# Kernel optimization log

Measured on AMD Instinct MI355X. Metric: run time of the kernel, lower is better.

## Reference

```python
import jax, jax.numpy as jnp
import numpy as np

B, T = 32, 64
I, O, H = 64, 64, 512
N, W = 128, 64           # memory slots, slot width
IF = 3 * W + 6           # interface size


def setup_inputs() -> dict:
    key = jax.random.key(0)
    ks = jax.random.split(key, 6)
    s = 0.05
    return {
        "x": jax.random.normal(ks[0], (B, T, I), jnp.float32),
        "W_ih": jax.random.normal(ks[1], (4 * H, I + W), jnp.float32) * s,
        "W_hh": jax.random.normal(ks[2], (4 * H, H), jnp.float32) * s,
        "b_ih": jnp.zeros((4 * H,), jnp.float32),
        "b_hh": jnp.zeros((4 * H,), jnp.float32),
        "W_if": jax.random.normal(ks[3], (IF, H), jnp.float32) * s,
        "b_if": jnp.zeros((IF,), jnp.float32),
        "W_out": jax.random.normal(ks[4], (O, H + W), jnp.float32) * s,
        "b_out": jnp.zeros((O,), jnp.float32),
    }


def reference(x, W_ih, W_hh, b_ih, b_hh, W_if, b_if, W_out, b_out):
    Bb, Tt, _ = x.shape
    dt = x.dtype
    eye = jnp.eye(N, dtype=dt)
    batch_idx = jnp.arange(Bb)[:, None]

    def step(carry, x_t):
        h, c, mem, usage, prec, link, rw, rvec = carry
        # --- LSTM controller (PyTorch gate order i,f,g,o) ---
        inp = jnp.concatenate([x_t, rvec], axis=-1)
        gates = inp @ W_ih.T + h @ W_hh.T + b_ih + b_hh
        i_g, f_g, g_g, o_g = jnp.split(gates, 4, axis=-1)
        c = jax.nn.sigmoid(f_g) * c + jax.nn.sigmoid(i_g) * jnp.tanh(g_g)
        h = jax.nn.sigmoid(o_g) * jnp.tanh(c)
        itf = h @ W_if.T + b_if
        # --- parse interface ---
        erase = jax.nn.sigmoid(itf[:, :W])
        wvec = itf[:, W:2 * W]
        wg = jax.nn.sigmoid(itf[:, 2 * W])
        ag = jax.nn.sigmoid(itf[:, 2 * W + 1])
        rstr = jnp.log1p(jnp.exp(itf[:, 3 * W + 2]))  # softplus
        # --- allocation weighting (sort usage asc, shifted cumprod, scatter) ---
        idx = jnp.argsort(usage, axis=-1)
        usage_sorted = jnp.take_along_axis(usage, idx, axis=-1)
        cprod = jnp.cumprod(usage_sorted, axis=-1)
        cprod = jnp.concatenate([jnp.ones((Bb, 1), dt), cprod[:, :-1]], axis=-1)
        alloc_in_order = (1.0 - usage_sorted) * cprod
        alloc = jnp.zeros_like(usage).at[batch_idx, idx].set(alloc_in_order)
        ww = wg[:, None] * ag[:, None] * alloc  # [B,N]
        # --- erase + add write ---
        mem = mem * (1.0 - ww[:, :, None] * erase[:, None, :]) + ww[:, :, None] * wvec[:, None, :]
        usage = usage + (1.0 - usage) * ww
        # --- temporal link / precedence ---
        ww_ij = ww[:, :, None] + ww[:, None, :]
        link = (1.0 - ww_ij) * link + prec[:, :, None] * ww[:, None, :]
        link = link * (1.0 - eye)
        prec = (1.0 - ww.sum(-1, keepdims=True)) * prec + ww
        # --- read weights (NOTE: source uses itf[:, :W] as read key) ---
        rmode = jax.nn.softmax(itf[:, -3:], axis=-1)
        rkey = itf[:, :W]
        dot = jnp.einsum('bw,bnw->bn', rkey, mem)
        kn = jnp.linalg.norm(rkey, axis=-1, keepdims=True) + 1e-8
        mn = jnp.linalg.norm(mem, axis=-1) + 1e-8
        cw = jax.nn.softmax(dot / (kn * mn) * rstr[:, None], axis=-1)
        bw = jnp.einsum('bnm,bn->bm', link, rw)   # link^T @ rw
        fw = jnp.einsum('bnm,bm->bn', link, rw)   # link @ rw
        wts = rmode[:, 0:1] * bw + rmode[:, 1:2] * fw + rmode[:, 2:3] * cw + 1e-8
        wts = wts / wts.sum(-1, keepdims=True)
        rvec = jnp.einsum('bn,bnw->bw', wts, mem)
        out = jnp.concatenate([h, rvec], axis=-1) @ W_out.T + b_out
        return (h, c, mem, usage, prec, link, wts, rvec), out

    z = lambda *s: jnp.zeros(s, dt)
    carry0 = (z(Bb, H), z(Bb, H), z(Bb, N, W), z(Bb, N), z(Bb, N), z(Bb, N, N), z(Bb, N), z(Bb, W))
    _, outs = jax.lax.scan(step, carry0, jnp.swapaxes(x, 0, 1))
    return jnp.swapaxes(outs, 0, 1)  # [B,T,O]
```

## Files before the change

kernel.cpp:

```cpp
#include <hip/hip_runtime.h>
#include <math.h>

#define Bb 32
#define Tt 64
#define Ii 64
#define Oo 64
#define Hh 512
#define Nn 128
#define Wd 64
#define IFs 198
#define KV 640
#define G4 2048

#define NP1 128
#define NWG 160
#define NT 512

#define P2_MEM    0
#define P2_H      8320
#define P2_SCR    8896
#define P2_ITF    10944
#define P2_ERASE  11168
#define P2_WVEC   11232
#define P2_USAGE  11296
#define P2_PREC   11424
#define P2_RW     11552
#define P2_WW     11680
#define P2_SCAN   11808
#define P2_SS     11936
#define P2_SCAL   12064
#define P2_BIF    12080
#define P2_ALLOC  12304
#define P1_WIF    0
#define P1_BS     13464
#define P1_V      13720
#define P1_CC     15016
#define P1_HSL    15144
#define P1_PACC   15272
#define SMEM_FLOATS 23592
#define SMEM_BYTES (SMEM_FLOATS * 4)

#define S_WWSUM 0

__device__ __align__(16) float g_WT[KV * G4];
__device__ __align__(16) float g_bsum[G4];
typedef unsigned long long u64;
__device__ u64 g_h64[2 * Bb * Hh];
__device__ u64 g_rv64[Bb * Wd];
__device__ u64 g_if64[Bb * 8 * 200];

__device__ __forceinline__ float sigf(float v) { return 1.f / (1.f + expf(-v)); }

__device__ __forceinline__ u64 ldrelax(const u64* p) {
  return __hip_atomic_load(p, __ATOMIC_RELAXED, __HIP_MEMORY_SCOPE_AGENT);
}
__device__ __forceinline__ void tstore(u64* p, unsigned tag, float v) {
  u64 val = ((u64)tag << 32) | (u64)__float_as_uint(v);
  __hip_atomic_store(p, val, __ATOMIC_RELAXED, __HIP_MEMORY_SCOPE_AGENT);
}
__device__ __forceinline__ float fixwait(const u64* p, u64 v, unsigned tag) {
  while ((unsigned)(v >> 32) != tag) {
    __builtin_amdgcn_s_sleep(1);
    v = ldrelax(p);
  }
  return __uint_as_float((unsigned)(v & 0xffffffffu));
}

#define TIN 512
__global__ __launch_bounds__(TIN) void dnc_init(const float* __restrict__ W_ih,
                                                const float* __restrict__ W_hh,
                                                const float* __restrict__ b_ih,
                                                const float* __restrict__ b_hh) {
  __shared__ float tile[64][65];
  const int tid = threadIdx.x;
  int i0 = blockIdx.x * blockDim.x + tid;
  int st = gridDim.x * blockDim.x;
  for (int idx = i0; idx < G4; idx += st) g_bsum[idx] = b_ih[idx] + b_hh[idx];
  for (int idx = i0; idx < 2 * Bb * Hh; idx += st) g_h64[idx] = 0ull;
  for (int idx = i0; idx < Bb * Wd; idx += st) g_rv64[idx] = 0ull;
  for (int idx = i0; idx < Bb * 8 * 200; idx += st) g_if64[idx] = 0ull;

  for (int tileId = blockIdx.x; tileId < 320; tileId += gridDim.x) {
    int tc = tileId >> 5, tj = tileId & 31;
    for (int k = tid; k < 64 * 64; k += TIN) {
      int r = k >> 6, cl = k & 63;
      int j = tj * 64 + r, c = tc * 64 + cl;
      tile[r][cl] = (c < 128) ? W_ih[j * 128 + c] : W_hh[j * 512 + (c - 128)];
    }
    __syncthreads();
    for (int k = tid; k < 64 * 64; k += TIN) {
      int cl = k >> 6, rjj = k & 63;
      int c = tc * 64 + cl;
      int rp = (c < 128) ? (512 + c) : (c - 128);
      g_WT[(size_t)rp * G4 + tj * 64 + rjj] = tile[rjj][cl];
    }
    __syncthreads();
  }
}

__global__ __launch_bounds__(NT) void dnc_main(const float* __restrict__ x,
                                               const float* __restrict__ W_if,
                                               const float* __restrict__ b_if,
                                               const float* __restrict__ W_out,
                                               const float* __restrict__ b_out,
                                               float* __restrict__ out) {
  extern __shared__ float sm[];
  const int tid = threadIdx.x;
  const int wg = blockIdx.x;

  if (wg < NP1) {
    const int jb = wg & 7;
    const int bb = wg >> 3;
    const int b0 = bb * 2;
    for (int i = tid; i < IFs * 64; i += NT) {
      int o = i >> 6, c = i & 63;
      sm[P1_WIF + o * 68 + c] = W_if[(size_t)o * Hh + jb * 64 + c];
    }
    if (tid < 64) {
      int gq = tid >> 4, m = tid & 15;
      ((float4*)(sm + P1_BS))[tid] = ((const float4*)g_bsum)[gq * 128 + jb * 16 + m];
    }
    if (tid < 128) sm[P1_CC + tid] = 0.f;
    __syncthreads();

    for (int t = 0; t < Tt; ++t) {
      {
        const u64* hsrc = g_h64 + (size_t)((t + 1) & 1) * (Bb * Hh);
        const int u = tid;
        const u64* a0 = hsrc + (size_t)b0 * Hh + u;
        const u64* a1 = hsrc + (size_t)(b0 + 1) * Hh + u;
        u64 v0 = ldrelax(a0), v1 = ldrelax(a1);
        float2 hh;
        hh.x = fixwait(a0, v0, (unsigned)t);
        hh.y = fixwait(a1, v1, (unsigned)t);
        *(float2*)(sm + P1_V + u * 2) = hh;
        if (tid < 128) {
          const int bl2 = tid >> 6, i = tid & 63;
          float xv = x[((size_t)(b0 + bl2) * Tt + t) * Ii + i];
          sm[P1_V + (512 + i) * 2 + bl2] = xv;
        }
      }
      __syncthreads();

      {
        const int fg = tid & 31, ks = tid >> 5;
        const int fcolA = ((fg >> 4) * 128) + jb * 16 + (fg & 15);
        const float* v2 = sm + P1_V + ks * 80;
        const float4* wpA = (const float4*)g_WT + (size_t)(ks * 40) * 512 + fcolA;
        if (ks >= 14) {
          const int j = tid & 63;
          const u64* r0 = g_rv64 + (size_t)b0 * Wd + j;
          const u64* r1 = g_rv64 + (size_t)(b0 + 1) * Wd + j;
          u64 u0 = ldrelax(r0), u1 = ldrelax(r1);
          float2 rv;
          rv.x = fixwait(r0, u0, (unsigned)t);
          rv.y = fixwait(r1, u1, (unsigned)t);
          *(float2*)(sm + P1_V + (576 + j) * 2) = rv;
        }
        float4 aA0 = {0.f, 0.f, 0.f, 0.f}, aA1 = {0.f, 0.f, 0.f, 0.f};
        float4 aB0 = {0.f, 0.f, 0.f, 0.f}, aB1 = {0.f, 0.f, 0.f, 0.f};
#pragma unroll 4
        for (int r = 0; r < 40; ++r) {
          float4 wA = wpA[(size_t)r * 512];
          float4 wB = wpA[(size_t)r * 512 + 256];
          float2 vv = *(const float2*)(v2 + r * 2);
          aA0.x += wA.x * vv.x; aA0.y += wA.y * vv.x; aA0.z += wA.z * vv.x; aA0.w += wA.w * vv.x;
          aA1.x += wA.x * vv.y; aA1.y += wA.y * vv.y; aA1.z += wA.z * vv.y; aA1.w += wA.w * vv.y;
          aB0.x += wB.x * vv.x; aB0.y += wB.y * vv.x; aB0.z += wB.z * vv.x; aB0.w += wB.w * vv.x;
          aB1.x += wB.x * vv.y; aB1.y += wB.y * vv.y; aB1.z += wB.z * vv.y; aB1.w += wB.w * vv.y;
        }
        float4* pacc = (float4*)(sm + P1_PACC);
        pacc[(ks * 2 + 0) * 65 + fg] = aA0;
        pacc[(ks * 2 + 1) * 65 + fg] = aA1;
        pacc[(ks * 2 + 0) * 65 + fg + 32] = aB0;
        pacc[(ks * 2 + 1) * 65 + fg + 32] = aB1;
      }
      __syncthreads();
      if (tid < 128) {
        const int bl = tid >> 6, l = tid & 63;
        const float* pb = sm + P1_PACC + bl * 260 + l;
        float gv0 = 0.f, gv1 = 0.f, gv2 = 0.f, gv3 = 0.f;
#pragma unroll
        for (int ks = 0; ks < 16; ++ks) {
          const float* pk = pb + ks * 520;
          gv0 += pk[0];
          gv1 += pk[64];
          gv2 += pk[128];
          gv3 += pk[192];
        }
        float ig = gv0 + sm[P1_BS + l];
        float fg = gv1 + sm[P1_BS + 64 + l];
        float gg = gv2 + sm[P1_BS + 128 + l];
        float og = gv3 + sm[P1_BS + 192 + l];
        float co = sm[P1_CC + bl * 64 + l];
        float cn = sigf(fg) * co + sigf(ig) * tanhf(gg);
        float hn = sigf(og) * tanhf(cn);
        sm[P1_CC + bl * 64 + l] = cn;
        sm[P1_HSL + bl * 64 + l] = hn;
        tstore(g_h64 + (size_t)(t & 1) * (Bb * Hh) + (size_t)(b0 + bl) * Hh + jb * 64 + l,
               (unsigned)(t + 1), hn);
      }
      __syncthreads();
      if (tid < 2 * IFs) {
        const int o = tid >> 1, bl = tid & 1;
        const float4* wr = (const float4*)(sm + P1_WIF + o * 68);
        const float4* h4 = (const float4*)(sm + P1_HSL + bl * 64);
        float acc = 0.f;
#pragma unroll 8
        for (int c4 = 0; c4 < 16; ++c4) {
          float4 w = wr[c4]; float4 h = h4[c4];
          acc += w.x * h.x + w.y * h.y + w.z * h.z + w.w * h.w;
        }
        tstore(g_if64 + ((size_t)(b0 + bl) * 8 + jb) * 200 + o, (unsigned)(t + 1), acc);
      }
    }
  } else {
    const int b = wg - NP1;
    float* SCR = sm + P2_SCR;
    float regL[32], regLT[32];
#pragma unroll
    for (int k = 0; k < 32; ++k) { regL[k] = 0.f; regLT[k] = 0.f; }
    for (int i = tid; i < Nn * 65; i += NT) sm[P2_MEM + i] = 0.f;
    if (tid < 128) { sm[P2_USAGE + tid] = 0.f; sm[P2_PREC + tid] = 0.f; sm[P2_RW + tid] = 0.f; }
    if (tid < IFs) sm[P2_BIF + tid] = b_if[tid];
    __syncthreads();
    if (tid < 64) {
      const int li = tid, i0 = 2 * li, i1 = i0 + 1;
      float u0 = sm[P2_USAGE + i0], u1 = sm[P2_USAGE + i1];
      int r0 = 0, r1 = 0;
      for (int jc = 0; jc < 32; ++jc) {
        float4 uj4 = *(const float4*)(sm + P2_USAGE + jc * 4);
#pragma unroll
        for (int e = 0; e < 4; ++e) {
          float uj = (&uj4.x)[e];
          int j = jc * 4 + e;
          r0 += (uj < u0 || (uj == u0 && j < i0)) ? 1 : 0;
          r1 += (uj < u1 || (uj == u1 && j < i1)) ? 1 : 0;
        }
      }
      sm[P2_SS + r0] = u0;
      sm[P2_SS + r1] = u1;
      float s0 = sm[P2_SS + i0], s1 = sm[P2_SS + i1];
      float p = s0 * s1;
#pragma unroll
      for (int off = 1; off < 64; off <<= 1) {
        float v = __shfl_up(p, off, 64);
        if (li >= off) p *= v;
      }
      float E = __shfl_up(p, 1, 64);
      if (li == 0) E = 1.f;
      sm[P2_SCAN + i0] = E * s0;
      sm[P2_SCAN + i1] = E * s0 * s1;
      float ex0 = (r0 > 0) ? sm[P2_SCAN + r0 - 1] : 1.f;
      float ex1 = (r1 > 0) ? sm[P2_SCAN + r1 - 1] : 1.f;
      sm[P2_ALLOC + i0] = (1.f - u0) * ex0;
      sm[P2_ALLOC + i1] = (1.f - u1) * ex1;
    }
    __syncthreads();

    for (int t = 0; t < Tt; ++t) {
      if (tid < 2 * IFs) {
        const int o = tid >> 1, hf = tid & 1;
        const u64* src = g_if64 + ((size_t)b * 8 + hf * 4) * 200 + o;
        u64 a0 = ldrelax(src), a1 = ldrelax(src + 200),
            a2 = ldrelax(src + 400), a3 = ldrelax(src + 600);
        float s = fixwait(src, a0, (unsigned)(t + 1))
                + fixwait(src + 200, a1, (unsigned)(t + 1))
                + fixwait(src + 400, a2, (unsigned)(t + 1))
                + fixwait(src + 600, a3, (unsigned)(t + 1));
        s += __shfl_xor(s, 1, 64);
        if (hf == 0) sm[P2_ITF + o] = s + sm[P2_BIF + o];
      }
      __syncthreads();
      float kn_r = 0.f, rstr_r = 0.f, rm0_r = 0.f, rm1_r = 0.f, rm2_r = 0.f;
      if (tid < 64) {
        const int li = tid, i0 = 2 * li, i1 = i0 + 1;
        float wgag = sigf(sm[P2_ITF + 128]) * sigf(sm[P2_ITF + 129]);
        float rs = sm[P2_ITF + 194];
        rstr_r = (rs > 20.f) ? rs : log1pf(expf(rs));
        float m0 = sm[P2_ITF + 195], m1 = sm[P2_ITF + 196], m2 = sm[P2_ITF + 197];
        float mx = fmaxf(m0, fmaxf(m1, m2));
        float e0 = expf(m0 - mx), e1 = expf(m1 - mx), e2 = expf(m2 - mx);
        float es = e0 + e1 + e2;
        rm0_r = e0 / es; rm1_r = e1 / es; rm2_r = e2 / es;
        float rk = sm[P2_ITF + li];
        sm[P2_ERASE + li] = sigf(rk);
        sm[P2_WVEC + li] = sm[P2_ITF + 64 + li];
        float sq = rk * rk;
#pragma unroll
        for (int off = 32; off > 0; off >>= 1) sq += __shfl_xor(sq, off, 64);
        kn_r = sqrtf(sq) + 1e-8f;
        float u0 = sm[P2_USAGE + i0], u1 = sm[P2_USAGE + i1];
        float w0 = wgag * sm[P2_ALLOC + i0];
        float w1 = wgag * sm[P2_ALLOC + i1];
        sm[P2_WW + i0] = w0; sm[P2_WW + i1] = w1;
        sm[P2_USAGE + i0] = u0 + (1.f - u0) * w0;
        sm[P2_USAGE + i1] = u1 + (1.f - u1) * w1;
        float wws = w0 + w1;
#pragma unroll
        for (int off = 32; off > 0; off >>= 1) wws += __shfl_xor(wws, off, 64);
        if (li == 0) sm[P2_SCAL + S_WWSUM] = wws;
      }
      __syncthreads();
      {
        const int n = tid & 127, ws = tid >> 7;
        float4 er[4], wv[4], kf[4];
#pragma unroll
        for (int r = 0; r < 4; ++r) {
          er[r] = *(const float4*)(sm + P2_ERASE + ws * 16 + r * 4);
          wv[r] = *(const float4*)(sm + P2_WVEC + ws * 16 + r * 4);
          kf[r] = *(const float4*)(sm + P2_ITF + ws * 16 + r * 4);
        }
        float wwn = sm[P2_WW + n];
        float dotp = 0.f, mnp = 0.f;
        const int base = P2_MEM + n * 65 + ws * 16;
#pragma unroll
        for (int q = 0; q < 16; ++q) {
          float m = sm[base + q];
          float ee = (&er[q >> 2].x)[q & 3];
          float vv = (&wv[q >> 2].x)[q & 3];
          float kk = (&kf[q >> 2].x)[q & 3];
          m = m * (1.f - wwn * ee) + wwn * vv;
          sm[base + q] = m;
          dotp += kk * m;
          mnp += m * m;
        }
        SCR[ws * 128 + n] = dotp;
        SCR[512 + ws * 128 + n] = mnp;
        const int m = n, ns = ws;
        float wwm = wwn;
        float prn = sm[P2_PREC + m];
        float bwp = 0.f, fwp = 0.f;
#pragma unroll
        for (int kq = 0; kq < 8; ++kq) {
          float4 ww4 = *(const float4*)(sm + P2_WW + ns * 32 + kq * 4);
          float4 pr4 = *(const float4*)(sm + P2_PREC + ns * 32 + kq * 4);
          float4 rw4 = *(const float4*)(sm + P2_RW + ns * 32 + kq * 4);
#pragma unroll
          for (int e = 0; e < 4; ++e) {
            int k = kq * 4 + e;
            int nn = ns * 32 + k;
            float wwo = (&ww4.x)[e];
            float pro = (&pr4.x)[e];
            float rwo = (&rw4.x)[e];
            float L = regL[k];
            L = (1.f - wwo - wwm) * L + pro * wwm;
            if (nn == m) L = 0.f;
            regL[k] = L;
            bwp += L * rwo;
            float LT = regLT[k];
            LT = (1.f - wwm - wwo) * LT + prn * wwo;
            if (nn == m) LT = 0.f;
            regLT[k] = LT;
            fwp += LT * rwo;
          }
        }
        SCR[1024 + ns * 128 + m] = bwp;
        SCR[1536 + ns * 128 + m] = fwp;
      }
      __syncthreads();
      if (tid < 64) {
        int i0 = 2 * tid, i1 = i0 + 1;
        float d0 = SCR[i0] + SCR[128 + i0] + SCR[256 + i0] + SCR[384 + i0];
        float d1 = SCR[i1] + SCR[128 + i1] + SCR[256 + i1] + SCR[384 + i1];
        float mn0 = sqrtf(SCR[512 + i0] + SCR[640 + i0] + SCR[768 + i0] + SCR[896 + i0]) + 1e-8f;
        float mn1 = sqrtf(SCR[512 + i1] + SCR[640 + i1] + SCR[768 + i1] + SCR[896 + i1]) + 1e-8f;
        float bw0 = SCR[1024 + i0] + SCR[1152 + i0] + SCR[1280 + i0] + SCR[1408 + i0];
        float bw1 = SCR[1024 + i1] + SCR[1152 + i1] + SCR[1280 + i1] + SCR[1408 + i1];
        float fw0 = SCR[1536 + i0] + SCR[1664 + i0] + SCR[1792 + i0] + SCR[1920 + i0];
        float fw1 = SCR[1536 + i1] + SCR[1664 + i1] + SCR[1792 + i1] + SCR[1920 + i1];
        float q0 = d0 / (kn_r * mn0) * rstr_r;
        float q1 = d1 / (kn_r * mn1) * rstr_r;
        float mx = fmaxf(q0, q1);
#pragma unroll
        for (int off = 32; off > 0; off >>= 1) mx = fmaxf(mx, __shfl_xor(mx, off, 64));
        float e0 = expf(q0 - mx), e1 = expf(q1 - mx);
        float es = e0 + e1;
#pragma unroll
        for (int off = 32; off > 0; off >>= 1) es += __shfl_xor(es, off, 64);
        float wv0 = rm0_r * bw0 + rm1_r * fw0 + rm2_r * (e0 / es) + 1e-8f;
        float wv1 = rm0_r * bw1 + rm1_r * fw1 + rm2_r * (e1 / es) + 1e-8f;
        float wsum = wv0 + wv1;
#pragma unroll
        for (int off = 32; off > 0; off >>= 1) wsum += __shfl_xor(wsum, off, 64);
        sm[P2_RW + i0] = wv0 / wsum;
        sm[P2_RW + i1] = wv1 / wsum;
      }
      __syncthreads();
      {
        const int w = tid & 63, ns8 = tid >> 6;
        float4 rw4[4];
#pragma unroll
        for (int r = 0; r < 4; ++r)
          rw4[r] = *(const float4*)(sm + P2_RW + ns8 * 16 + r * 4);
        float p = 0.f;
#pragma unroll
        for (int k = 0; k < 16; ++k)
          p += (&rw4[k >> 2].x)[k & 3] * sm[P2_MEM + (ns8 * 16 + k) * 65 + w];
        SCR[ns8 * 64 + w] = p;
      }
      __syncthreads();
      if (tid < 64) {
        float r = 0.f;
#pragma unroll
        for (int s2 = 0; s2 < 8; ++s2) r += SCR[s2 * 64 + tid];
        sm[P2_H + 512 + tid] = r;
        tstore(g_rv64 + (size_t)b * Wd + tid, (unsigned)(t + 1), r);
      } else if (tid < 320) {
        const int idx = tid - 64;
        const u64* hsrc = g_h64 + (size_t)(t & 1) * (Bb * Hh) + (size_t)b * Hh;
        const u64* a0 = hsrc + idx * 2;
        const u64* a1 = hsrc + idx * 2 + 1;
        u64 v0 = ldrelax(a0), v1 = ldrelax(a1);
        sm[P2_H + idx * 2] = fixwait(a0, v0, (unsigned)(t + 1));
        sm[P2_H + idx * 2 + 1] = fixwait(a1, v1, (unsigned)(t + 1));
      } else if (tid < 384) {
        const int li = tid - 320, i0 = 2 * li, i1 = i0 + 1;
        float u0 = sm[P2_USAGE + i0], u1 = sm[P2_USAGE + i1];
        int r0 = 0, r1 = 0;
        for (int jc = 0; jc < 32; ++jc) {
          float4 uj4 = *(const float4*)(sm + P2_USAGE + jc * 4);
#pragma unroll
          for (int e = 0; e < 4; ++e) {
            float uj = (&uj4.x)[e];
            int j = jc * 4 + e;
            r0 += (uj < u0 || (uj == u0 && j < i0)) ? 1 : 0;
            r1 += (uj < u1 || (uj == u1 && j < i1)) ? 1 : 0;
          }
        }
        sm[P2_SS + r0] = u0;
        sm[P2_SS + r1] = u1;
        float s0 = sm[P2_SS + i0], s1 = sm[P2_SS + i1];
        float p = s0 * s1;
#pragma unroll
        for (int off = 1; off < 64; off <<= 1) {
          float v = __shfl_up(p, off, 64);
          if (li >= off) p *= v;
        }
        float E = __shfl_up(p, 1, 64);
        if (li == 0) E = 1.f;
        sm[P2_SCAN + i0] = E * s0;
        sm[P2_SCAN + i1] = E * s0 * s1;
        float ex0 = (r0 > 0) ? sm[P2_SCAN + r0 - 1] : 1.f;
        float ex1 = (r1 > 0) ? sm[P2_SCAN + r1 - 1] : 1.f;
        sm[P2_ALLOC + i0] = (1.f - u0) * ex0;
        sm[P2_ALLOC + i1] = (1.f - u1) * ex1;
      } else {
        const int n = tid - 384;
        float wws = sm[P2_SCAL + S_WWSUM];
        sm[P2_PREC + n] = (1.f - wws) * sm[P2_PREC + n] + sm[P2_WW + n];
      }
      __syncthreads();
      {
        const int o = tid >> 3, seg = tid & 7;
        const float4* wrow = (const float4*)(W_out + (size_t)o * 576) + seg * 18;
        const float4* hb = (const float4*)(sm + P2_H) + seg * 18;
        float p = 0.f;
#pragma unroll
        for (int q = 0; q < 18; ++q) {
          float4 w = wrow[q]; float4 h = hb[q];
          p += w.x * h.x + w.y * h.y + w.z * h.z + w.w * h.w;
        }
        p += __shfl_down(p, 4, 8);
        p += __shfl_down(p, 2, 8);
        p += __shfl_down(p, 1, 8);
        if (seg == 0) out[((size_t)b * Tt + t) * Oo + o] = p + b_out[o];
      }
    }
  }
}

extern "C" void kernel_launch(void* const* d_in, const int* in_sizes, int n_in,
                              void* d_out, int out_size, void* d_ws, size_t ws_size,
                              hipStream_t stream) {
  (void)in_sizes; (void)n_in; (void)d_ws; (void)ws_size; (void)out_size;
  const float* x    = (const float*)d_in[0];
  const float* W_ih = (const float*)d_in[1];
  const float* W_hh = (const float*)d_in[2];
  const float* b_ih = (const float*)d_in[3];
  const float* b_hh = (const float*)d_in[4];
  const float* W_if = (const float*)d_in[5];
  const float* b_if = (const float*)d_in[6];
  const float* W_out = (const float*)d_in[7];
  const float* b_out = (const float*)d_in[8];
  float* out = (float*)d_out;

  dnc_init<<<320, TIN, 0, stream>>>(W_ih, W_hh, b_ih, b_hh);

  hipFuncSetAttribute((const void*)dnc_main,
                      hipFuncAttributeMaxDynamicSharedMemorySize, SMEM_BYTES);

  void* args[] = {(void*)&x, (void*)&W_if, (void*)&b_if,
                  (void*)&W_out, (void*)&b_out, (void*)&out};
  hipLaunchCooperativeKernel((void*)dnc_main, dim3(NWG), dim3(NT), args,
                             SMEM_BYTES, stream);
}
```

Baseline: 873.5 us.

## Merge LSTM and memory stages into uniform per-batch workgroups with redundant memory updates

Replaces the split of 128 LSTM workgroups plus 32 memory workgroups with 256 uniform workgroups. Each handles one batch element and one slice of hidden units, and each redundantly keeps its own copy of the DNC memory, link and usage state. This removes the cross-workgroup read-vector handoff (g_rv64) and the dedicated memory stage from the critical path. Each group now gathers the interface vector from the 8 partial sums and runs the full memory update locally, and the output projection is deferred by one step and spread across groups. In exchange it does 8x redundant memory work, uses more shared memory per group (launch bounds set to 2 groups per CU), and reuses each weight load for only one batch row instead of two.

```diff
diff --git a/kernel.cpp b/kernel.cpp
--- a/kernel.cpp
+++ b/kernel.cpp
@@ -12,41 +12,36 @@
 #define KV 640
 #define G4 2048
 
-#define NP1 128
-#define NWG 160
+#define NWG 256
 #define NT 512
 
-#define P2_MEM    0
-#define P2_H      8320
-#define P2_SCR    8896
-#define P2_ITF    10944
-#define P2_ERASE  11168
-#define P2_WVEC   11232
-#define P2_USAGE  11296
-#define P2_PREC   11424
-#define P2_RW     11552
-#define P2_WW     11680
-#define P2_SCAN   11808
-#define P2_SS     11936
-#define P2_SCAL   12064
-#define P2_BIF    12080
-#define P2_ALLOC  12304
-#define P1_WIF    0
-#define P1_BS     13464
-#define P1_V      13720
-#define P1_CC     15016
-#define P1_HSL    15144
-#define P1_PACC   15272
-#define SMEM_FLOATS 23592
+#define L_WIF    0
+#define L_BS     13464
+#define L_V      13720
+#define L_CC     14360
+#define L_HSL    14424
+#define L_BIF    14488
+#define L_ITF    14712
+#define L_ERASE  14936
+#define L_WVEC   15000
+#define L_USAGE  15064
+#define L_PREC   15192
+#define L_RW     15320
+#define L_WW     15448
+#define L_SCAN   15576
+#define L_SS     15704
+#define L_ALLOC  15832
+#define L_SCAL   15960
+#define L_SCR    15976
+#define L_PACC   18024
+#define L_MEM    22184
+#define SMEM_FLOATS 30504
 #define SMEM_BYTES (SMEM_FLOATS * 4)
-
-#define S_WWSUM 0
 
 __device__ __align__(16) float g_WT[KV * G4];
 __device__ __align__(16) float g_bsum[G4];
 typedef unsigned long long u64;
 __device__ u64 g_h64[2 * Bb * Hh];
-__device__ u64 g_rv64[Bb * Wd];
 __device__ u64 g_if64[Bb * 8 * 200];
 
 __device__ __forceinline__ float sigf(float v) { return 1.f / (1.f + expf(-v)); }
@@ -77,7 +72,6 @@
   int st = gridDim.x * blockDim.x;
   for (int idx = i0; idx < G4; idx += st) g_bsum[idx] = b_ih[idx] + b_hh[idx];
   for (int idx = i0; idx < 2 * Bb * Hh; idx += st) g_h64[idx] = 0ull;
-  for (int idx = i0; idx < Bb * Wd; idx += st) g_rv64[idx] = 0ull;
   for (int idx = i0; idx < Bb * 8 * 200; idx += st) g_if64[idx] = 0ull;
 
   for (int tileId = blockIdx.x; tileId < 320; tileId += gridDim.x) {
@@ -98,138 +92,319 @@
   }
 }
 
-__global__ __launch_bounds__(NT) void dnc_main(const float* __restrict__ x,
-                                               const float* __restrict__ W_if,
-                                               const float* __restrict__ b_if,
-                                               const float* __restrict__ W_out,
-                                               const float* __restrict__ b_out,
-                                               float* __restrict__ out) {
+__global__ __launch_bounds__(NT, 2) void dnc_main(const float* __restrict__ x,
+                                                  const float* __restrict__ W_if,
+                                                  const float* __restrict__ b_if,
+                                                  const float* __restrict__ W_out,
+                                                  const float* __restrict__ b_out,
+                                                  float* __restrict__ out) {
   extern __shared__ float sm[];
   const int tid = threadIdx.x;
   const int wg = blockIdx.x;
-
-  if (wg < NP1) {
-    const int jb = wg & 7;
-    const int bb = wg >> 3;
-    const int b0 = bb * 2;
-    for (int i = tid; i < IFs * 64; i += NT) {
-      int o = i >> 6, c = i & 63;
-      sm[P1_WIF + o * 68 + c] = W_if[(size_t)o * Hh + jb * 64 + c];
-    }
+  const int jb = wg & 7;
+  const int b = wg >> 3;
+
+  float regL[32], regLT[32];
+#pragma unroll
+  for (int k = 0; k < 32; ++k) { regL[k] = 0.f; regLT[k] = 0.f; }
+
+  for (int i = tid; i < IFs * 64; i += NT) {
+    int o = i >> 6, c = i & 63;
+    sm[L_WIF + o * 68 + c] = W_if[(size_t)o * Hh + jb * 64 + c];
+  }
+  if (tid < 64) {
+    int gq = tid >> 4, m = tid & 15;
+    ((float4*)(sm + L_BS))[tid] = ((const float4*)g_bsum)[gq * 128 + jb * 16 + m];
+    sm[L_CC + tid] = 0.f;
+    sm[L_V + 576 + tid] = 0.f;
+  }
+  if (tid < IFs) sm[L_BIF + tid] = b_if[tid];
+  if (tid < 128) {
+    sm[L_USAGE + tid] = 0.f;
+    sm[L_PREC + tid] = 0.f;
+    sm[L_RW + tid] = 0.f;
+  }
+  for (int i = tid; i < Nn * 65; i += NT) sm[L_MEM + i] = 0.f;
+  __syncthreads();
+  if (tid < 64) {
+    const int li = tid, i0 = 2 * li, i1 = i0 + 1;
+    float u0 = sm[L_USAGE + i0], u1 = sm[L_USAGE + i1];
+    int r0 = 0, r1 = 0;
+    for (int jc = 0; jc < 32; ++jc) {
+      float4 uj4 = *(const float4*)(sm + L_USAGE + jc * 4);
+#pragma unroll
+      for (int e = 0; e < 4; ++e) {
+        float uj = (&uj4.x)[e];
+        int j = jc * 4 + e;
+        r0 += (uj < u0 || (uj == u0 && j < i0)) ? 1 : 0;
+        r1 += (uj < u1 || (uj == u1 && j < i1)) ? 1 : 0;
+      }
+    }
+    sm[L_SS + r0] = u0;
+    sm[L_SS + r1] = u1;
+    float s0 = sm[L_SS + i0], s1 = sm[L_SS + i1];
+    float p = s0 * s1;
+#pragma unroll
+    for (int off = 1; off < 64; off <<= 1) {
+      float v = __shfl_up(p, off, 64);
+      if (li >= off) p *= v;
+    }
+    float E = __shfl_up(p, 1, 64);
+    if (li == 0) E = 1.f;
+    sm[L_SCAN + i0] = E * s0;
+    sm[L_SCAN + i1] = E * s0 * s1;
+    float ex0 = (r0 > 0) ? sm[L_SCAN + r0 - 1] : 1.f;
+    float ex1 = (r1 > 0) ? sm[L_SCAN + r1 - 1] : 1.f;
+    sm[L_ALLOC + i0] = (1.f - u0) * ex0;
+    sm[L_ALLOC + i1] = (1.f - u1) * ex1;
+  }
+  __syncthreads();
+
+  for (int t = 0; t < Tt; ++t) {
+    {
+      const u64* a0 = g_h64 + (size_t)((t + 1) & 1) * (Bb * Hh) + (size_t)b * Hh + tid;
+      u64 v0 = ldrelax(a0);
+      sm[L_V + tid] = fixwait(a0, v0, (unsigned)t);
+      if (tid < 64) sm[L_V + 512 + tid] = x[((size_t)b * Tt + t) * Ii + tid];
+    }
+    __syncthreads();
+    {
+      const int fg = tid & 31, ks = tid >> 5;
+      const int fcolA = ((fg >> 4) * 128) + jb * 16 + (fg & 15);
+      const float* va = sm + L_V + ks * 40;
+      const float4* wpA = (const float4*)g_WT + (size_t)(ks * 40) * 512 + fcolA;
+      float4 aA = {0.f, 0.f, 0.f, 0.f}, aB = {0.f, 0.f, 0.f, 0.f};
+#pragma unroll 4
+      for (int r = 0; r < 40; ++r) {
+        float4 wA = wpA[(size_t)r * 512];
+        float4 wB = wpA[(size_t)r * 512 + 256];
+        float fv = va[r];
+        aA.x += wA.x * fv; aA.y += wA.y * fv; aA.z += wA.z * fv; aA.w += wA.w * fv;
+        aB.x += wB.x * fv; aB.y += wB.y * fv; aB.z += wB.z * fv; aB.w += wB.w * fv;
+      }
+      float4* pacc = (float4*)(sm + L_PACC);
+      pacc[ks * 65 + fg] = aA;
+      pacc[ks * 65 + fg + 32] = aB;
+    }
+    __syncthreads();
     if (tid < 64) {
-      int gq = tid >> 4, m = tid & 15;
-      ((float4*)(sm + P1_BS))[tid] = ((const float4*)g_bsum)[gq * 128 + jb * 16 + m];
-    }
-    if (tid < 128) sm[P1_CC + tid] = 0.f;
-    __syncthreads();
-
-    for (int t = 0; t < Tt; ++t) {
-      {
-        const u64* hsrc = g_h64 + (size_t)((t + 1) & 1) * (Bb * Hh);
-        const int u = tid;
-        const u64* a0 = hsrc + (size_t)b0 * Hh + u;
-        const u64* a1 = hsrc + (size_t)(b0 + 1) * Hh + u;
-        u64 v0 = ldrelax(a0), v1 = ldrelax(a1);
-        float2 hh;
-        hh.x = fixwait(a0, v0, (unsigned)t);
-        hh.y = fixwait(a1, v1, (unsigned)t);
-        *(float2*)(sm + P1_V + u * 2) = hh;
-        if (tid < 128) {
-          const int bl2 = tid >> 6, i = tid & 63;
-          float xv = x[((size_t)(b0 + bl2) * Tt + t) * Ii + i];
-          sm[P1_V + (512 + i) * 2 + bl2] = xv;
-        }
-      }
-      __syncthreads();
-
-      {
-        const int fg = tid & 31, ks = tid >> 5;
-        const int fcolA = ((fg >> 4) * 128) + jb * 16 + (fg & 15);
-        const float* v2 = sm + P1_V + ks * 80;
-        const float4* wpA = (const float4*)g_WT + (size_t)(ks * 40) * 512 + fcolA;
-        if (ks >= 14) {
-          const int j = tid & 63;
-          const u64* r0 = g_rv64 + (size_t)b0 * Wd + j;
-          const u64* r1 = g_rv64 + (size_t)(b0 + 1) * Wd + j;
-          u64 u0 = ldrelax(r0), u1 = ldrelax(r1);
-          float2 rv;
-          rv.x = fixwait(r0, u0, (unsigned)t);
-          rv.y = fixwait(r1, u1, (unsigned)t);
-          *(float2*)(sm + P1_V + (576 + j) * 2) = rv;
-        }
-        float4 aA0 = {0.f, 0.f, 0.f, 0.f}, aA1 = {0.f, 0.f, 0.f, 0.f};
-        float4 aB0 = {0.f, 0.f, 0.f, 0.f}, aB1 = {0.f, 0.f, 0.f, 0.f};
-#pragma unroll 4
-        for (int r = 0; r < 40; ++r) {
-          float4 wA = wpA[(size_t)r * 512];
-          float4 wB = wpA[(size_t)r * 512 + 256];
-          float2 vv = *(const float2*)(v2 + r * 2);
-          aA0.x += wA.x * vv.x; aA0.y += wA.y * vv.x; aA0.z += wA.z * vv.x; aA0.w += wA.w * vv.x;
-          aA1.x += wA.x * vv.y; aA1.y += wA.y * vv.y; aA1.z += wA.z * vv.y; aA1.w += wA.w * vv.y;
-          aB0.x += wB.x * vv.x; aB0.y += wB.y * vv.x; aB0.z += wB.z * vv.x; aB0.w += wB.w * vv.x;
-          aB1.x += wB.x * vv.y; aB1.y += wB.y * vv.y; aB1.z += wB.z * vv.y; aB1.w += wB.w * vv.y;
-        }
-        float4* pacc = (float4*)(sm + P1_PACC);
-        pacc[(ks * 2 + 0) * 65 + fg] = aA0;
-        pacc[(ks * 2 + 1) * 65 + fg] = aA1;
-        pacc[(ks * 2 + 0) * 65 + fg + 32] = aB0;
-        pacc[(ks * 2 + 1) * 65 + fg + 32] = aB1;
-      }
-      __syncthreads();
-      if (tid < 128) {
-        const int bl = tid >> 6, l = tid & 63;
-        const float* pb = sm + P1_PACC + bl * 260 + l;
-        float gv0 = 0.f, gv1 = 0.f, gv2 = 0.f, gv3 = 0.f;
-#pragma unroll
-        for (int ks = 0; ks < 16; ++ks) {
-          const float* pk = pb + ks * 520;
-          gv0 += pk[0];
-          gv1 += pk[64];
-          gv2 += pk[128];
-          gv3 += pk[192];
-        }
-        float ig = gv0 + sm[P1_BS + l];
-        float fg = gv1 + sm[P1_BS + 64 + l];
-        float gg = gv2 + sm[P1_BS + 128 + l];
-        float og = gv3 + sm[P1_BS + 192 + l];
-        float co = sm[P1_CC + bl * 64 + l];
-        float cn = sigf(fg) * co + sigf(ig) * tanhf(gg);
-        float hn = sigf(og) * tanhf(cn);
-        sm[P1_CC + bl * 64 + l] = cn;
-        sm[P1_HSL + bl * 64 + l] = hn;
-        tstore(g_h64 + (size_t)(t & 1) * (Bb * Hh) + (size_t)(b0 + bl) * Hh + jb * 64 + l,
-               (unsigned)(t + 1), hn);
-      }
-      __syncthreads();
-      if (tid < 2 * IFs) {
-        const int o = tid >> 1, bl = tid & 1;
-        const float4* wr = (const float4*)(sm + P1_WIF + o * 68);
-        const float4* h4 = (const float4*)(sm + P1_HSL + bl * 64);
-        float acc = 0.f;
-#pragma unroll 8
-        for (int c4 = 0; c4 < 16; ++c4) {
-          float4 w = wr[c4]; float4 h = h4[c4];
-          acc += w.x * h.x + w.y * h.y + w.z * h.z + w.w * h.w;
-        }
-        tstore(g_if64 + ((size_t)(b0 + bl) * 8 + jb) * 200 + o, (unsigned)(t + 1), acc);
-      }
-    }
-  } else {
-    const int b = wg - NP1;
-    float* SCR = sm + P2_SCR;
-    float regL[32], regLT[32];
-#pragma unroll
-    for (int k = 0; k < 32; ++k) { regL[k] = 0.f; regLT[k] = 0.f; }
-    for (int i = tid; i < Nn * 65; i += NT) sm[P2_MEM + i] = 0.f;
-    if (tid < 128) { sm[P2_USAGE + tid] = 0.f; sm[P2_PREC + tid] = 0.f; sm[P2_RW + tid] = 0.f; }
-    if (tid < IFs) sm[P2_BIF + tid] = b_if[tid];
-    __syncthreads();
+      const int l = tid;
+      const float* pb = sm + L_PACC + l;
+      float gv0 = 0.f, gv1 = 0.f, gv2 = 0.f, gv3 = 0.f;
+#pragma unroll
+      for (int ks = 0; ks < 16; ++ks) {
+        const float* pk = pb + ks * 260;
+        gv0 += pk[0];
+        gv1 += pk[64];
+        gv2 += pk[128];
+        gv3 += pk[192];
+      }
+      float ig = gv0 + sm[L_BS + l];
+      float fg = gv1 + sm[L_BS + 64 + l];
+      float gg = gv2 + sm[L_BS + 128 + l];
+      float og = gv3 + sm[L_BS + 192 + l];
+      float co = sm[L_CC + l];
+      float cn = sigf(fg) * co + sigf(ig) * tanhf(gg);
+      float hn = sigf(og) * tanhf(cn);
+      sm[L_CC + l] = cn;
+      sm[L_HSL + l] = hn;
+      tstore(g_h64 + (size_t)(t & 1) * (Bb * Hh) + (size_t)b * Hh + jb * 64 + l,
+             (unsigned)(t + 1), hn);
+    }
+    __syncthreads();
+    if (tid < 2 * IFs) {
+      const int o = tid >> 1, hf = tid & 1;
+      const float4* wr = (const float4*)(sm + L_WIF + o * 68) + hf * 8;
+      const float4* h4 = (const float4*)(sm + L_HSL) + hf * 8;
+      float acc = 0.f;
+#pragma unroll
+      for (int c4 = 0; c4 < 8; ++c4) {
+        float4 w = wr[c4]; float4 h = h4[c4];
+        acc += w.x * h.x + w.y * h.y + w.z * h.z + w.w * h.w;
+      }
+      acc += __shfl_xor(acc, 1, 64);
+      if (hf == 0)
+        tstore(g_if64 + ((size_t)b * 8 + jb) * 200 + o, (unsigned)(t + 1), acc);
+    }
+    const u64 *pp0, *pp1, *pp2, *pp3;
+    u64 pv0 = 0, pv1 = 0, pv2 = 0, pv3 = 0;
+    if (tid < 2 * IFs) {
+      const int o = tid >> 1, hf = tid & 1;
+      const u64* base = g_if64 + (size_t)b * 8 * 200 + (size_t)hf * 4 * 200 + o;
+      pp0 = base; pp1 = base + 200; pp2 = base + 400; pp3 = base + 600;
+      pv0 = ldrelax(pp0); pv1 = ldrelax(pp1); pv2 = ldrelax(pp2); pv3 = ldrelax(pp3);
+    }
+    if (t > 0 && tid >= 448) {
+      const int o8 = (tid - 448) >> 3, seg = tid & 7;
+      const int o = jb * 8 + o8;
+      const float4* w4 = (const float4*)(W_out + (size_t)o * 576) + seg * 18;
+      float p = 0.f;
+#pragma unroll
+      for (int q = 0; q < 18; ++q) {
+        float4 w = w4[q];
+        int v = seg * 72 + q * 4;
+        int r0 = (v < 512) ? v : v + 64;
+        p += w.x * sm[L_V + r0] + w.y * sm[L_V + r0 + 1]
+           + w.z * sm[L_V + r0 + 2] + w.w * sm[L_V + r0 + 3];
+      }
+      p += __shfl_down(p, 4, 8);
+      p += __shfl_down(p, 2, 8);
+      p += __shfl_down(p, 1, 8);
+      if (seg == 0) out[((size_t)b * Tt + (t - 1)) * Oo + o] = p + b_out[o];
+    }
+    if (tid < 2 * IFs) {
+      const int o = tid >> 1, hf = tid & 1;
+      float s = fixwait(pp0, pv0, (unsigned)(t + 1))
+              + fixwait(pp1, pv1, (unsigned)(t + 1))
+              + fixwait(pp2, pv2, (unsigned)(t + 1))
+              + fixwait(pp3, pv3, (unsigned)(t + 1));
+      s += __shfl_xor(s, 1, 64);
+      if (hf == 0) sm[L_ITF + o] = s + sm[L_BIF + o];
+    }
+    __syncthreads();
+    float kn_r = 0.f, rstr_r = 0.f, rm0_r = 0.f, rm1_r = 0.f, rm2_r = 0.f;
     if (tid < 64) {
       const int li = tid, i0 = 2 * li, i1 = i0 + 1;
-      float u0 = sm[P2_USAGE + i0], u1 = sm[P2_USAGE + i1];
+      float wgag = sigf(sm[L_ITF + 128]) * sigf(sm[L_ITF + 129]);
+      float rs = sm[L_ITF + 194];
+      rstr_r = (rs > 20.f) ? rs : log1pf(expf(rs));
+      float m0 = sm[L_ITF + 195], m1 = sm[L_ITF + 196], m2 = sm[L_ITF + 197];
+      float mx = fmaxf(m0, fmaxf(m1, m2));
+      float e0 = expf(m0 - mx), e1 = expf(m1 - mx), e2 = expf(m2 - mx);
+      float es = e0 + e1 + e2;
+      rm0_r = e0 / es; rm1_r = e1 / es; rm2_r = e2 / es;
+      float rk = sm[L_ITF + li];
+      sm[L_ERASE + li] = sigf(rk);
+      sm[L_WVEC + li] = sm[L_ITF + 64 + li];
+      float sq = rk * rk;
+#pragma unroll
+      for (int off = 32; off > 0; off >>= 1) sq += __shfl_xor(sq, off, 64);
+      kn_r = sqrtf(sq) + 1e-8f;
+      float u0 = sm[L_USAGE + i0], u1 = sm[L_USAGE + i1];
+      float w0 = wgag * sm[L_ALLOC + i0];
+      float w1 = wgag * sm[L_ALLOC + i1];
+      sm[L_WW + i0] = w0; sm[L_WW + i1] = w1;
+      sm[L_USAGE + i0] = u0 + (1.f - u0) * w0;
+      sm[L_USAGE + i1] = u1 + (1.f - u1) * w1;
+      float wws = w0 + w1;
+#pragma unroll
+      for (int off = 32; off > 0; off >>= 1) wws += __shfl_xor(wws, off, 64);
+      if (li == 0) sm[L_SCAL] = wws;
+    }
+    __syncthreads();
+    {
+      float* SCR = sm + L_SCR;
+      const int n = tid & 127, ws = tid >> 7;
+      float4 er[4], wv[4], kf[4];
+#pragma unroll
+      for (int r = 0; r < 4; ++r) {
+        er[r] = *(const float4*)(sm + L_ERASE + ws * 16 + r * 4);
+        wv[r] = *(const float4*)(sm + L_WVEC + ws * 16 + r * 4);
+        kf[r] = *(const float4*)(sm + L_ITF + ws * 16 + r * 4);
+      }
+      float wwn = sm[L_WW + n];
+      float dotp = 0.f, mnp = 0.f;
+      const int base = L_MEM + n * 65 + ws * 16;
+#pragma unroll
+      for (int q = 0; q < 16; ++q) {
+        float m = sm[base + q];
+        float ee = (&er[q >> 2].x)[q & 3];
+        float vv = (&wv[q >> 2].x)[q & 3];
+        float kk = (&kf[q >> 2].x)[q & 3];
+        m = m * (1.f - wwn * ee) + wwn * vv;
+        sm[base + q] = m;
+        dotp += kk * m;
+        mnp += m * m;
+      }
+      SCR[ws * 128 + n] = dotp;
+      SCR[512 + ws * 128 + n] = mnp;
+      const int m = n, ns = ws;
+      float wwm = wwn;
+      float prn = sm[L_PREC + m];
+      float bwp = 0.f, fwp = 0.f;
+#pragma unroll
+      for (int kq = 0; kq < 8; ++kq) {
+        float4 ww4 = *(const float4*)(sm + L_WW + ns * 32 + kq * 4);
+        float4 pr4 = *(const float4*)(sm + L_PREC + ns * 32 + kq * 4);
+        float4 rw4 = *(const float4*)(sm + L_RW + ns * 32 + kq * 4);
+#pragma unroll
+        for (int e = 0; e < 4; ++e) {
+          int k = kq * 4 + e;
+          int nn = ns * 32 + k;
+          float wwo = (&ww4.x)[e];
+          float pro = (&pr4.x)[e];
+          float rwo = (&rw4.x)[e];
+          float L = regL[k];
+          L = (1.f - wwo - wwm) * L + pro * wwm;
+          if (nn == m) L = 0.f;
+          regL[k] = L;
+          bwp += L * rwo;
+          float LT = regLT[k];
+          LT = (1.f - wwm - wwo) * LT + prn * wwo;
+          if (nn == m) LT = 0.f;
+          regLT[k] = LT;
+          fwp += LT * rwo;
+        }
+      }
+      SCR[1024 + ns * 128 + m] = bwp;
+      SCR[1536 + ns * 128 + m] = fwp;
+    }
+    __syncthreads();
+    if (tid < 64) {
+      float* SCR = sm + L_SCR;
+      int i0 = 2 * tid, i1 = i0 + 1;
+      float d0 = SCR[i0] + SCR[128 + i0] + SCR[256 + i0] + SCR[384 + i0];
+      float d1 = SCR[i1] + SCR[128 + i1] + SCR[256 + i1] + SCR[384 + i1];
+      float mn0 = sqrtf(SCR[512 + i0] + SCR[640 + i0] + SCR[768 + i0] + SCR[896 + i0]) + 1e-8f;
+      float mn1 = sqrtf(SCR[512 + i1] + SCR[640 + i1] + SCR[768 + i1] + SCR[896 + i1]) + 1e-8f;
+      float bw0 = SCR[1024 + i0] + SCR[1152 + i0] + SCR[1280 + i0] + SCR[1408 + i0];
+      float bw1 = SCR[1024 + i1] + SCR[1152 + i1] + SCR[1280 + i1] + SCR[1408 + i1];
+      float fw0 = SCR[1536 + i0] + SCR[1664 + i0] + SCR[1792 + i0] + SCR[1920 + i0];
+      float fw1 = SCR[1536 + i1] + SCR[1664 + i1] + SCR[1792 + i1] + SCR[1920 + i1];
+      float q0 = d0 / (kn_r * mn0) * rstr_r;
+      float q1 = d1 / (kn_r * mn1) * rstr_r;
+      float mx = fmaxf(q0, q1);
+#pragma unroll
+      for (int off = 32; off > 0; off >>= 1) mx = fmaxf(mx, __shfl_xor(mx, off, 64));
+      float e0 = expf(q0 - mx), e1 = expf(q1 - mx);
+      float es = e0 + e1;
+#pragma unroll
+      for (int off = 32; off > 0; off >>= 1) es += __shfl_xor(es, off, 64);
+      float wv0 = rm0_r * bw0 + rm1_r * fw0 + rm2_r * (e0 / es) + 1e-8f;
+      float wv1 = rm0_r * bw1 + rm1_r * fw1 + rm2_r * (e1 / es) + 1e-8f;
+      float wsum = wv0 + wv1;
+#pragma unroll
+      for (int off = 32; off > 0; off >>= 1) wsum += __shfl_xor(wsum, off, 64);
+      sm[L_RW + i0] = wv0 / wsum;
+      sm[L_RW + i1] = wv1 / wsum;
+    }
+    __syncthreads();
+    {
+      float* SCR = sm + L_SCR;
+      const int w = tid & 63, ns8 = tid >> 6;
+      float4 rw4[4];
+#pragma unroll
+      for (int r = 0; r < 4; ++r)
+        rw4[r] = *(const float4*)(sm + L_RW + ns8 * 16 + r * 4);
+      float p = 0.f;
+#pragma unroll
+      for (int k = 0; k < 16; ++k)
+        p += (&rw4[k >> 2].x)[k & 3] * sm[L_MEM + (ns8 * 16 + k) * 65 + w];
+      SCR[ns8 * 64 + w] = p;
+    }
+    __syncthreads();
+    if (tid < 64) {
+      const float* SCR = sm + L_SCR;
+      float r = 0.f;
+#pragma unroll
+      for (int s2 = 0; s2 < 8; ++s2) r += SCR[s2 * 64 + tid];
+      sm[L_V + 576 + tid] = r;
+    } else if (tid < 128) {
+      const int li = tid - 64, i0 = 2 * li, i1 = i0 + 1;
+      float u0 = sm[L_USAGE + i0], u1 = sm[L_USAGE + i1];
       int r0 = 0, r1 = 0;
       for (int jc = 0; jc < 32; ++jc) {
-        float4 uj4 = *(const float4*)(sm + P2_USAGE + jc * 4);
+        float4 uj4 = *(const float4*)(sm + L_USAGE + jc * 4);
 #pragma unroll
         for (int e = 0; e < 4; ++e) {
           float uj = (&uj4.x)[e];
@@ -238,9 +413,9 @@
           r1 += (uj < u1 || (uj == u1 && j < i1)) ? 1 : 0;
         }
       }
-      sm[P2_SS + r0] = u0;
-      sm[P2_SS + r1] = u1;
-      float s0 = sm[P2_SS + i0], s1 = sm[P2_SS + i1];
+      sm[L_SS + r0] = u0;
+      sm[L_SS + r1] = u1;
+      float s0 = sm[L_SS + i0], s1 = sm[L_SS + i1];
       float p = s0 * s1;
 #pragma unroll
       for (int off = 1; off < 64; off <<= 1) {
@@ -249,224 +424,42 @@
       }
       float E = __shfl_up(p, 1, 64);
       if (li == 0) E = 1.f;
-      sm[P2_SCAN + i0] = E * s0;
-      sm[P2_SCAN + i1] = E * s0 * s1;
-      float ex0 = (r0 > 0) ? sm[P2_SCAN + r0 - 1] : 1.f;
-      float ex1 = (r1 > 0) ? sm[P2_SCAN + r1 - 1] : 1.f;
-      sm[P2_ALLOC + i0] = (1.f - u0) * ex0;
-      sm[P2_ALLOC + i1] = (1.f - u1) * ex1;
-    }
-    __syncthreads();
-
-    for (int t = 0; t < Tt; ++t) {
-      if (tid < 2 * IFs) {
-        const int o = tid >> 1, hf = tid & 1;
-        const u64* src = g_if64 + ((size_t)b * 8 + hf * 4) * 200 + o;
-        u64 a0 = ldrelax(src), a1 = ldrelax(src + 200),
-            a2 = ldrelax(src + 400), a3 = ldrelax(src + 600);
-        float s = fixwait(src, a0, (unsigned)(t + 1))
-                + fixwait(src + 200, a1, (unsigned)(t + 1))
-                + fixwait(src + 400, a2, (unsigned)(t + 1))
-                + fixwait(src + 600, a3, (unsigned)(t + 1));
-        s += __shfl_xor(s, 1, 64);
-        if (hf == 0) sm[P2_ITF + o] = s + sm[P2_BIF + o];
-      }
-      __syncthreads();
-      float kn_r = 0.f, rstr_r = 0.f, rm0_r = 0.f, rm1_r = 0.f, rm2_r = 0.f;
-      if (tid < 64) {
-        const int li = tid, i0 = 2 * li, i1 = i0 + 1;
-        float wgag = sigf(sm[P2_ITF + 128]) * sigf(sm[P2_ITF + 129]);
-        float rs = sm[P2_ITF + 194];
-        rstr_r = (rs > 20.f) ? rs : log1pf(expf(rs));
-        float m0 = sm[P2_ITF + 195], m1 = sm[P2_ITF + 196], m2 = sm[P2_ITF + 197];
-        float mx = fmaxf(m0, fmaxf(m1, m2));
-        float e0 = expf(m0 - mx), e1 = expf(m1 - mx), e2 = expf(m2 - mx);
-        float es = e0 + e1 + e2;
-        rm0_r = e0 / es; rm1_r = e1 / es; rm2_r = e2 / es;
-        float rk = sm[P2_ITF + li];
-        sm[P2_ERASE + li] = sigf(rk);
-        sm[P2_WVEC + li] = sm[P2_ITF + 64 + li];
-        float sq = rk * rk;
-#pragma unroll
-        for (int off = 32; off > 0; off >>= 1) sq += __shfl_xor(sq, off, 64);
-        kn_r = sqrtf(sq) + 1e-8f;
-        float u0 = sm[P2_USAGE + i0], u1 = sm[P2_USAGE + i1];
-        float w0 = wgag * sm[P2_ALLOC + i0];
-        float w1 = wgag * sm[P2_ALLOC + i1];
-        sm[P2_WW + i0] = w0; sm[P2_WW + i1] = w1;
-        sm[P2_USAGE + i0] = u0 + (1.f - u0) * w0;
-        sm[P2_USAGE + i1] = u1 + (1.f - u1) * w1;
-        float wws = w0 + w1;
-#pragma unroll
-        for (int off = 32; off > 0; off >>= 1) wws += __shfl_xor(wws, off, 64);
-        if (li == 0) sm[P2_SCAL + S_WWSUM] = wws;
-      }
-      __syncthreads();
-      {
-        const int n = tid & 127, ws = tid >> 7;
-        float4 er[4], wv[4], kf[4];
-#pragma unroll
-        for (int r = 0; r < 4; ++r) {
-          er[r] = *(const float4*)(sm + P2_ERASE + ws * 16 + r * 4);
-          wv[r] = *(const float4*)(sm + P2_WVEC + ws * 16 + r * 4);
-          kf[r] = *(const float4*)(sm + P2_ITF + ws * 16 + r * 4);
-        }
-        float wwn = sm[P2_WW + n];
-        float dotp = 0.f, mnp = 0.f;
-        const int base = P2_MEM + n * 65 + ws * 16;
-#pragma unroll
-        for (int q = 0; q < 16; ++q) {
-          float m = sm[base + q];
-          float ee = (&er[q >> 2].x)[q & 3];
-          float vv = (&wv[q >> 2].x)[q & 3];
-          float kk = (&kf[q >> 2].x)[q & 3];
-          m = m * (1.f - wwn * ee) + wwn * vv;
-          sm[base + q] = m;
-          dotp += kk * m;
-          mnp += m * m;
-        }
-        SCR[ws * 128 + n] = dotp;
-        SCR[512 + ws * 128 + n] = mnp;
-        const int m = n, ns = ws;
-        float wwm = wwn;
-        float prn = sm[P2_PREC + m];
-        float bwp = 0.f, fwp = 0.f;
-#pragma unroll
-        for (int kq = 0; kq < 8; ++kq) {
-          float4 ww4 = *(const float4*)(sm + P2_WW + ns * 32 + kq * 4);
-          float4 pr4 = *(const float4*)(sm + P2_PREC + ns * 32 + kq * 4);
-          float4 rw4 = *(const float4*)(sm + P2_RW + ns * 32 + kq * 4);
-#pragma unroll
-          for (int e = 0; e < 4; ++e) {
-            int k = kq * 4 + e;
-            int nn = ns * 32 + k;
-            float wwo = (&ww4.x)[e];
-            float pro = (&pr4.x)[e];
-            float rwo = (&rw4.x)[e];
-            float L = regL[k];
-            L = (1.f - wwo - wwm) * L + pro * wwm;
-            if (nn == m) L = 0.f;
-            regL[k] = L;
-            bwp += L * rwo;
-            float LT = regLT[k];
-            LT = (1.f - wwm - wwo) * LT + prn * wwo;
-            if (nn == m) LT = 0.f;
-            regLT[k] = LT;
-            fwp += LT * rwo;
-          }
-        }
-        SCR[1024 + ns * 128 + m] = bwp;
-        SCR[1536 + ns * 128 + m] = fwp;
-      }
-      __syncthreads();
-      if (tid < 64) {
-        int i0 = 2 * tid, i1 = i0 + 1;
-        float d0 = SCR[i0] + SCR[128 + i0] + SCR[256 + i0] + SCR[384 + i0];
-        float d1 = SCR[i1] + SCR[128 + i1] + SCR[256 + i1] + SCR[384 + i1];
-        float mn0 = sqrtf(SCR[512 + i0] + SCR[640 + i0] + SCR[768 + i0] + SCR[896 + i0]) + 1e-8f;
-        float mn1 = sqrtf(SCR[512 + i1] + SCR[640 + i1] + SCR[768 + i1] + SCR[896 + i1]) + 1e-8f;
-        float bw0 = SCR[1024 + i0] + SCR[1152 + i0] + SCR[1280 + i0] + SCR[1408 + i0];
-        float bw1 = SCR[1024 + i1] + SCR[1152 + i1] + SCR[1280 + i1] + SCR[1408 + i1];
-        float fw0 = SCR[1536 + i0] + SCR[1664 + i0] + SCR[1792 + i0] + SCR[1920 + i0];
-        float fw1 = SCR[1536 + i1] + SCR[1664 + i1] + SCR[1792 + i1] + SCR[1920 + i1];
-        float q0 = d0 / (kn_r * mn0) * rstr_r;
-        float q1 = d1 / (kn_r * mn1) * rstr_r;
-        float mx = fmaxf(q0, q1);
-#pragma unroll
-        for (int off = 32; off > 0; off >>= 1) mx = fmaxf(mx, __shfl_xor(mx, off, 64));
-        float e0 = expf(q0 - mx), e1 = expf(q1 - mx);
-        float es = e0 + e1;
-#pragma unroll
-        for (int off = 32; off > 0; off >>= 1) es += __shfl_xor(es, off, 64);
-        float wv0 = rm0_r * bw0 + rm1_r * fw0 + rm2_r * (e0 / es) + 1e-8f;
-        float wv1 = rm0_r * bw1 + rm1_r * fw1 + rm2_r * (e1 / es) + 1e-8f;
-        float wsum = wv0 + wv1;
-#pragma unroll
-        for (int off = 32; off > 0; off >>= 1) wsum += __shfl_xor(wsum, off, 64);
-        sm[P2_RW + i0] = wv0 / wsum;
-        sm[P2_RW + i1] = wv1 / wsum;
-      }
-      __syncthreads();
-      {
-        const int w = tid & 63, ns8 = tid >> 6;
-        float4 rw4[4];
-#pragma unroll
-        for (int r = 0; r < 4; ++r)
-          rw4[r] = *(const float4*)(sm + P2_RW + ns8 * 16 + r * 4);
-        float p = 0.f;
-#pragma unroll
-        for (int k = 0; k < 16; ++k)
-          p += (&rw4[k >> 2].x)[k & 3] * sm[P2_MEM + (ns8 * 16 + k) * 65 + w];
-        SCR[ns8 * 64 + w] = p;
-      }
-      __syncthreads();
-      if (tid < 64) {
-        float r = 0.f;
-#pragma unroll
-        for (int s2 = 0; s2 < 8; ++s2) r += SCR[s2 * 64 + tid];
-        sm[P2_H + 512 + tid] = r;
-        tstore(g_rv64 + (size_t)b * Wd + tid, (unsigned)(t + 1), r);
-      } else if (tid < 320) {
-        const int idx = tid - 64;
-        const u64* hsrc = g_h64 + (size_t)(t & 1) * (Bb * Hh) + (size_t)b * Hh;
-        const u64* a0 = hsrc + idx * 2;
-        const u64* a1 = hsrc + idx * 2 + 1;
-        u64 v0 = ldrelax(a0), v1 = ldrelax(a1);
-        sm[P2_H + idx * 2] = fixwait(a0, v0, (unsigned)(t + 1));
-        sm[P2_H + idx * 2 + 1] = fixwait(a1, v1, (unsigned)(t + 1));
-      } else if (tid < 384) {
-        const int li = tid - 320, i0 = 2 * li, i1 = i0 + 1;
-        float u0 = sm[P2_USAGE + i0], u1 = sm[P2_USAGE + i1];
-        int r0 = 0, r1 = 0;
-        for (int jc = 0; jc < 32; ++jc) {
-          float4 uj4 = *(const float4*)(sm + P2_USAGE + jc * 4);
-#pragma unroll
-          for (int e = 0; e < 4; ++e) {
-            float uj = (&uj4.x)[e];
-            int j = jc * 4 + e;
-            r0 += (uj < u0 || (uj == u0 && j < i0)) ? 1 : 0;
-            r1 += (uj < u1 || (uj == u1 && j < i1)) ? 1 : 0;
-          }
-        }
-        sm[P2_SS + r0] = u0;
-        sm[P2_SS + r1] = u1;
-        float s0 = sm[P2_SS + i0], s1 = sm[P2_SS + i1];
-        float p = s0 * s1;
-#pragma unroll
-        for (int off = 1; off < 64; off <<= 1) {
-          float v = __shfl_up(p, off, 64);
-          if (li >= off) p *= v;
-        }
-        float E = __shfl_up(p, 1, 64);
-        if (li == 0) E = 1.f;
-        sm[P2_SCAN + i0] = E * s0;
-        sm[P2_SCAN + i1] = E * s0 * s1;
-        float ex0 = (r0 > 0) ? sm[P2_SCAN + r0 - 1] : 1.f;
-        float ex1 = (r1 > 0) ? sm[P2_SCAN + r1 - 1] : 1.f;
-        sm[P2_ALLOC + i0] = (1.f - u0) * ex0;
-        sm[P2_ALLOC + i1] = (1.f - u1) * ex1;
-      } else {
-        const int n = tid - 384;
-        float wws = sm[P2_SCAL + S_WWSUM];
-        sm[P2_PREC + n] = (1.f - wws) * sm[P2_PREC + n] + sm[P2_WW + n];
-      }
-      __syncthreads();
-      {
-        const int o = tid >> 3, seg = tid & 7;
-        const float4* wrow = (const float4*)(W_out + (size_t)o * 576) + seg * 18;
-        const float4* hb = (const float4*)(sm + P2_H) + seg * 18;
-        float p = 0.f;
-#pragma unroll
-        for (int q = 0; q < 18; ++q) {
-          float4 w = wrow[q]; float4 h = hb[q];
-          p += w.x * h.x + w.y * h.y + w.z * h.z + w.w * h.w;
-        }
-        p += __shfl_down(p, 4, 8);
-        p += __shfl_down(p, 2, 8);
-        p += __shfl_down(p, 1, 8);
-        if (seg == 0) out[((size_t)b * Tt + t) * Oo + o] = p + b_out[o];
-      }
-    }
+      sm[L_SCAN + i0] = E * s0;
+      sm[L_SCAN + i1] = E * s0 * s1;
+      float ex0 = (r0 > 0) ? sm[L_SCAN + r0 - 1] : 1.f;
+      float ex1 = (r1 > 0) ? sm[L_SCAN + r1 - 1] : 1.f;
+      sm[L_ALLOC + i0] = (1.f - u0) * ex0;
+      sm[L_ALLOC + i1] = (1.f - u1) * ex1;
+    } else if (tid < 256) {
+      const int n = tid - 128;
+      float wws = sm[L_SCAL];
+      sm[L_PREC + n] = (1.f - wws) * sm[L_PREC + n] + sm[L_WW + n];
+    }
+    __syncthreads();
+  }
+  {
+    const u64* a0 = g_h64 + (size_t)((Tt + 1) & 1) * (Bb * Hh) + (size_t)b * Hh + tid;
+    u64 v0 = ldrelax(a0);
+    sm[L_V + tid] = fixwait(a0, v0, (unsigned)Tt);
+  }
+  __syncthreads();
+  if (tid < 64) {
+    const int o8 = tid >> 3, seg = tid & 7;
+    const int o = jb * 8 + o8;
+    const float4* w4 = (const float4*)(W_out + (size_t)o * 576) + seg * 18;
+    float p = 0.f;
+#pragma unroll
+    for (int q = 0; q < 18; ++q) {
+      float4 w = w4[q];
+      int v = seg * 72 + q * 4;
+      int r0 = (v < 512) ? v : v + 64;
+      p += w.x * sm[L_V + r0] + w.y * sm[L_V + r0 + 1]
+         + w.z * sm[L_V + r0 + 2] + w.w * sm[L_V + r0 + 3];
+    }
+    p += __shfl_down(p, 4, 8);
+    p += __shfl_down(p, 2, 8);
+    p += __shfl_down(p, 1, 8);
+    if (seg == 0) out[((size_t)b * Tt + (Tt - 1)) * Oo + o] = p + b_out[o];
   }
 }
 
```

Result: slower. 1.644 ms (+88.2%).
